# Kernel optimization log

Measured on AMD Instinct MI355X. Metric: run time of the kernel, lower is better.

Reference implementation:

```python
import jax, jax.numpy as jnp
import numpy as np

DIM = 128
HEADS = 4
HEAD_DIM = DIM // HEADS
WS = (8, 8)
N = WS[0] * WS[1]
B = 4096
SCALE = HEAD_DIM ** -0.5


def _relative_position_index():
    # Swin-style relative position index, [N, N] int
    ch = np.arange(WS[0]); cw = np.arange(WS[1])
    coords = np.stack(np.meshgrid(ch, cw, indexing='ij'))          # [2, ws0, ws1]
    flat = coords.reshape(2, -1)                                    # [2, N]
    rel = flat[:, :, None] - flat[:, None, :]                       # [2, N, N]
    rel = rel.transpose(1, 2, 0)                                    # [N, N, 2]
    rel[:, :, 0] += WS[0] - 1
    rel[:, :, 1] += WS[1] - 1
    rel[:, :, 0] *= 2 * WS[1] - 1
    return jnp.asarray(rel.sum(-1))

REL_IDX = _relative_position_index()


def setup_inputs() -> dict:
    key = jax.random.key(0)
    ks = jax.random.split(key, 16)
    def lin(k, din, dout):
        return jax.random.normal(k, (din, dout), jnp.float32) * (din ** -0.5)
    return {
        'x': jax.random.normal(ks[0], (B, N, DIM), jnp.float32),
        'f': jax.random.normal(ks[1], (B, N, DIM), jnp.float32),
        'wq': lin(ks[2], DIM, DIM), 'bq': jnp.zeros((DIM,), jnp.float32),
        'wkv': lin(ks[3], DIM, 2 * DIM), 'bkv': jnp.zeros((2 * DIM,), jnp.float32),
        'wq_f': lin(ks[4], DIM, DIM), 'bq_f': jnp.zeros((DIM,), jnp.float32),
        'wkv_f': lin(ks[5], DIM, 2 * DIM), 'bkv_f': jnp.zeros((2 * DIM,), jnp.float32),
        'bias_table': jax.random.normal(ks[6], ((2 * WS[0] - 1) * (2 * WS[1] - 1), HEADS), jnp.float32) * 0.02,
        'wproj': lin(ks[7], DIM, DIM), 'bproj': jnp.zeros((DIM,), jnp.float32),
    }


def _qkv(t, wq, bq, wkv, bkv):
    Bn, Nn, C = t.shape
    q = (t @ wq + bq).reshape(Bn, Nn, HEADS, HEAD_DIM).transpose(0, 2, 1, 3)   # [B,H,N,D]
    kv = (t @ wkv + bkv).reshape(Bn, Nn, 2, HEADS, HEAD_DIM).transpose(2, 0, 3, 1, 4)
    return q, kv[0], kv[1]


def reference(x, f, wq, bq, wkv, bkv, wq_f, bq_f, wkv_f, bkv_f, bias_table, wproj, bproj):
    q, k, v = _qkv(x, wq, bq, wkv, bkv)
    attn = jnp.einsum('bhnd,bhmd->bhnm', q * SCALE, k)              # [B,H,N,N]
    q_f, k_f, _ = _qkv(f, wq_f, bq_f, wkv_f, bkv_f)
    attn_f = jnp.einsum('bhnd,bhmd->bhnm', q_f * SCALE, k_f)

    bias = bias_table[REL_IDX.reshape(-1)].reshape(N, N, HEADS)     # gather
    bias = bias.transpose(2, 0, 1)                                   # [H,N,N]
    ratio = attn.shape[-1] // bias.shape[-1]
    if ratio > 1:  # repeat last axis (no-op here since N == ws0*ws1)
        bias = jnp.repeat(bias, ratio, axis=-1)

    attn = (attn + bias[None]) * (attn_f + bias[None])               # joint modulation
    attn = jax.nn.softmax(attn, axis=-1)
    out = jnp.einsum('bhnm,bhmd->bhnd', attn, v)                     # [B,H,N,D]
    out = out.transpose(0, 2, 1, 3).reshape(x.shape[0], N, DIM)
    return out @ wproj + bproj
```

## Files before the change

### kernel.cpp

```cpp
#include <hip/hip_runtime.h>

typedef unsigned short u16;
typedef _Float16  f16x8  __attribute__((ext_vector_type(8)));
typedef _Float16  f16x4  __attribute__((ext_vector_type(4)));
typedef _Float16  f16x2  __attribute__((ext_vector_type(2)));
typedef float     f32x4  __attribute__((ext_vector_type(4)));

#define MFMA_F16(a,b,c)  __builtin_amdgcn_mfma_f32_16x16x32_f16(a,b,c,0,0,0)
#define PKRTZ(a,b) __builtin_bit_cast(f16x2, __builtin_amdgcn_cvt_pkrtz((a),(b)))

#define NTOK 64
#define DIM_ 128
#define SCALE_ 0.17677669529663687f

#define HREG 6784
#define KOFF 2304
#define VOFF 4608
#define SQK  36
#define SP   72
#define SAO  40
#define SVT  68
#define SMEM_U16 27136

__device__ __forceinline__ u16 f2h_u(float x) {
    _Float16 h = (_Float16)x;
    return __builtin_bit_cast(u16, h);
}

__global__ void wja_prep(const float* __restrict__ wq, const float* __restrict__ wkv,
                         const float* __restrict__ wq_f, const float* __restrict__ wkv_f,
                         const float* __restrict__ wproj, u16* __restrict__ ws)
{
    const int blk = blockIdx.x;
    const int l = threadIdx.x;
    const float* W; int ldw, colbase;
    if (blk < 32)       { W = wq;    ldw = 128; colbase = (blk      >> 2) * 16; }
    else if (blk < 96)  { W = wkv;   ldw = 256; colbase = ((blk- 32) >> 2) * 16; }
    else if (blk < 128) { W = wq_f;  ldw = 128; colbase = ((blk- 96) >> 2) * 16; }
    else if (blk < 160) { W = wkv_f; ldw = 256; colbase = ((blk-128) >> 2) * 16; }
    else                { W = wproj; ldw = 128; colbase = ((blk-160) >> 2) * 16; }
    const int ks = blk & 3;
    const int m = l & 15, g = l >> 4;
    u16* dst = ws + blk * 512 + l * 8;
    #pragma unroll
    for (int i = 0; i < 8; ++i)
        dst[i] = f2h_u(W[(size_t)(32*ks + 8*g + i) * ldw + colbase + m]);
}

__global__ __launch_bounds__(256, 2)
void wja_fused(
    const float* __restrict__ x, const float* __restrict__ f,
    const float* __restrict__ bq, const float* __restrict__ bkv,
    const float* __restrict__ bq_f, const float* __restrict__ bkv_f,
    const float* __restrict__ bproj, const float* __restrict__ btab,
    const u16* __restrict__ ws, float* __restrict__ out)
{
    __shared__ __align__(16) u16 smem[SMEM_U16];
    const int b    = blockIdx.x;
    const int tid  = threadIdx.x;
    const int w    = tid >> 6;
    const int lane = tid & 63;
    const int g    = lane >> 4;
    const int c    = lane & 15;
    const f32x4 zf4 = {0.f, 0.f, 0.f, 0.f};

    u16* const hb = smem + w * HREG;

    const float* const xb = x + (size_t)b * (NTOK * DIM_);
    const float* const fb = f + (size_t)b * (NTOK * DIM_);

    auto ldf16 = [](const float* p) -> f16x8 {
        f32x4 v0 = *(const f32x4*)p;
        f32x4 v1 = *(const f32x4*)(p + 4);
        struct Q { f16x2 a, b, c, d; } t;
        t.a = PKRTZ(v0[0], v0[1]);
        t.b = PKRTZ(v0[2], v0[3]);
        t.c = PKRTZ(v1[0], v1[1]);
        t.d = PKRTZ(v1[2], v1[3]);
        return __builtin_bit_cast(f16x8, t);
    };
    auto ldlds8 = [](const u16* p) -> f16x8 {
        struct P2 { f16x4 lo, hi; } t;
        t.lo = *(const f16x4*)p;
        t.hi = *(const f16x4*)(p + 4);
        return __builtin_bit_cast(f16x8, t);
    };

    f16x8 xfr[4], ffr[4];
    #pragma unroll
    for (int ks = 0; ks < 4; ++ks) {
        xfr[ks] = ldf16(xb + (16*w + c) * DIM_ + 32*ks + 8*g);
        ffr[ks] = ldf16(fb + (16*w + c) * DIM_ + 32*ks + 8*g);
    }

    auto gemmA = [&](const f16x8* afr, int wbase, const float* biasv, int which) {
        #pragma unroll
        for (int lct = 0; lct < 8; ++lct) {
            f32x4 acc = zf4;
            #pragma unroll
            for (int ks = 0; ks < 4; ++ks) {
                f16x8 bfr = *(const f16x8*)(ws + (wbase + 4*lct + ks) * 512 + lane * 8);
                acc = MFMA_F16(afr[ks], bfr, acc);
            }
            float bv = biasv[16*lct + c];
            const int hh = lct >> 1;
            const int cc = ((lct & 1) << 4) + c;
            if (which == 2) {
                struct H4 { f16x2 lo, hi; } t;
                t.lo = PKRTZ(acc[0] + bv, acc[1] + bv);
                t.hi = PKRTZ(acc[2] + bv, acc[3] + bv);
                *(f16x4*)(smem + hh*HREG + VOFF + cc*SVT + 16*w + 4*g) =
                    __builtin_bit_cast(f16x4, t);
            } else {
                const int base = hh*HREG + (which ? KOFF : 0);
                #pragma unroll
                for (int i = 0; i < 4; ++i)
                    smem[base + (16*w + 4*g + i)*SQK + cc] = f2h_u(acc[i] + bv);
            }
        }
    };

    gemmA(xfr,   0, bq,        0);
    gemmA(xfr,  32, bkv,       1);
    gemmA(xfr,  64, bkv + 128, 2);
    __syncthreads();

    f32x4 S[4][4];
    {
        f16x8 qfr[4], kfr[4];
        #pragma unroll
        for (int t = 0; t < 4; ++t) {
            qfr[t] = ldlds8(hb + (16*t + c) * SQK + 8*g);
            kfr[t] = ldlds8(hb + KOFF + (16*t + c) * SQK + 8*g);
        }
        #pragma unroll
        for (int mt = 0; mt < 4; ++mt)
            #pragma unroll
            for (int nt = 0; nt < 4; ++nt)
                S[mt][nt] = MFMA_F16(qfr[mt], kfr[nt], zf4);
    }
    __syncthreads();

    gemmA(ffr,  96, bq_f,  0);
    gemmA(ffr, 128, bkv_f, 1);
    __syncthreads();

    {
        f16x8 kfr[4];
        #pragma unroll
        for (int t = 0; t < 4; ++t)
            kfr[t] = ldlds8(hb + KOFF + (16*t + c) * SQK + 8*g);
        #pragma unroll
        for (int mt = 0; mt < 4; ++mt) {
            f16x8 qfr = ldlds8(hb + (16*mt + c) * SQK + 8*g);
            #pragma unroll
            for (int nt = 0; nt < 4; ++nt) {
                f32x4 sf = MFMA_F16(qfr, kfr[nt], zf4);
                int j = 16*nt + c;
                #pragma unroll
                for (int i = 0; i < 4; ++i) {
                    int r = 16*mt + 4*g + i;
                    int idx = ((r >> 3) - (j >> 3) + 7) * 15 + ((r & 7) - (j & 7) + 7);
                    float bv = btab[idx * 4 + w];
                    S[mt][nt][i] = (S[mt][nt][i] * SCALE_ + bv) * (sf[i] * SCALE_ + bv);
                }
            }
        }
    }

    float rinv[4][4];
    #pragma unroll
    for (int mt = 0; mt < 4; ++mt)
        #pragma unroll
        for (int i = 0; i < 4; ++i) {
            float m = fmaxf(fmaxf(S[mt][0][i], S[mt][1][i]), fmaxf(S[mt][2][i], S[mt][3][i]));
            #pragma unroll
            for (int d = 1; d < 16; d <<= 1) m = fmaxf(m, __shfl_xor(m, d));
            float s0 = 0.f;
            #pragma unroll
            for (int nt = 0; nt < 4; ++nt) {
                float e = __expf(S[mt][nt][i] - m);
                S[mt][nt][i] = e;
                s0 += e;
            }
            #pragma unroll
            for (int d = 1; d < 16; d <<= 1) s0 += __shfl_xor(s0, d);
            rinv[mt][i] = 1.0f / s0;
        }

    #pragma unroll
    for (int mt = 0; mt < 4; ++mt)
        #pragma unroll
        for (int nt = 0; nt < 4; ++nt)
            #pragma unroll
            for (int i = 0; i < 4; ++i)
                hb[(16*mt + 4*g + i) * SP + 16*nt + c] = f2h_u(S[mt][nt][i] * rinv[mt][i]);

    f32x4 O[4][2] = { { zf4, zf4 }, { zf4, zf4 }, { zf4, zf4 }, { zf4, zf4 } };
    #pragma unroll
    for (int ks = 0; ks < 2; ++ks) {
        f16x8 pfr[4], vfr[2];
        #pragma unroll
        for (int mt = 0; mt < 4; ++mt)
            pfr[mt] = *(const f16x8*)(hb + (16*mt + c) * SP + 32*ks + 8*g);
        #pragma unroll
        for (int nt = 0; nt < 2; ++nt)
            vfr[nt] = ldlds8(hb + VOFF + (16*nt + c) * SVT + 32*ks + 8*g);
        #pragma unroll
        for (int mt = 0; mt < 4; ++mt)
            #pragma unroll
            for (int nt = 0; nt < 2; ++nt)
                O[mt][nt] = MFMA_F16(pfr[mt], vfr[nt], O[mt][nt]);
    }

    #pragma unroll
    for (int mt = 0; mt < 4; ++mt)
        #pragma unroll
        for (int nt = 0; nt < 2; ++nt)
            #pragma unroll
            for (int i = 0; i < 4; ++i)
                hb[(16*mt + 4*g + i) * SAO + 16*nt + c] = f2h_u(O[mt][nt][i]);

    __syncthreads();

    f32x4 PO[4][2] = { { zf4, zf4 }, { zf4, zf4 }, { zf4, zf4 }, { zf4, zf4 } };
    #pragma unroll
    for (int ks = 0; ks < 4; ++ks) {
        const u16* ao = smem + ks * HREG;
        f16x8 afr[4];
        #pragma unroll
        for (int mt = 0; mt < 4; ++mt)
            afr[mt] = *(const f16x8*)(ao + (16*mt + c) * SAO + 8*g);
        #pragma unroll
        for (int lct = 0; lct < 2; ++lct) {
            f16x8 bfr = *(const f16x8*)(ws + (160 + (2*w + lct) * 4 + ks) * 512 + lane * 8);
            #pragma unroll
            for (int mt = 0; mt < 4; ++mt)
                PO[mt][lct] = MFMA_F16(afr[mt], bfr, PO[mt][lct]);
        }
    }

    float* const ob = out + (size_t)b * 8192;
    #pragma unroll
    for (int lct = 0; lct < 2; ++lct) {
        float bv = bproj[32*w + 16*lct + c];
        #pragma unroll
        for (int mt = 0; mt < 4; ++mt)
            #pragma unroll
            for (int i = 0; i < 4; ++i)
                ob[(16*mt + 4*g + i) * 128 + 32*w + 16*lct + c] = PO[mt][lct][i] + bv;
    }
}

extern "C" void kernel_launch(void* const* d_in, const int* in_sizes, int n_in,
                              void* d_out, int out_size, void* d_ws, size_t ws_size,
                              hipStream_t stream)
{
    const float* x     = (const float*)d_in[0];
    const float* f     = (const float*)d_in[1];
    const float* wq    = (const float*)d_in[2];
    const float* bq    = (const float*)d_in[3];
    const float* wkv   = (const float*)d_in[4];
    const float* bkv   = (const float*)d_in[5];
    const float* wq_f  = (const float*)d_in[6];
    const float* bq_f  = (const float*)d_in[7];
    const float* wkv_f = (const float*)d_in[8];
    const float* bkv_f = (const float*)d_in[9];
    const float* btab  = (const float*)d_in[10];
    const float* wproj = (const float*)d_in[11];
    const float* bproj = (const float*)d_in[12];
    u16* ws    = (u16*)d_ws;
    float* out = (float*)d_out;

    hipLaunchKernelGGL(wja_prep, dim3(192), dim3(64), 0, stream,
                       wq, wkv, wq_f, wkv_f, wproj, ws);
    hipLaunchKernelGGL(wja_fused, dim3(4096), dim3(256), 0, stream,
                       x, f, bq, bkv, bq_f, bkv_f, bproj, btab, ws, out);
}
```

Baseline: 195.2 us.

## Shrink LDS footprint by aliasing V with K and splitting PV into two halves

Cuts per-head shared memory from 6784 to 4480 halves by deferring the V projection until after the scores are done and storing V in the K region. The probability matrix is staged in two 32-column halves reusing the Q buffer instead of a full 64-wide buffer. K gets a new row stride of 34 and is read with 32-bit loads, aiming to reduce bank conflicts. The aim is higher occupancy from a smaller LDS footprint, at the cost of extra __syncthreads barriers and a later, serialized V GEMM.

After: 286.9 us. 47.0% more time.

```diff
diff --git a/kernel.cpp b/kernel.cpp
--- a/kernel.cpp
+++ b/kernel.cpp
@@ -13,14 +13,12 @@
 #define DIM_ 128
 #define SCALE_ 0.17677669529663687f
 
-#define HREG 6784
+#define HREG 4480
 #define KOFF 2304
-#define VOFF 4608
-#define SQK  36
-#define SP   72
-#define SAO  40
+#define SQ   36
+#define SK   34
 #define SVT  68
-#define SMEM_U16 27136
+#define SMEM_U16 17920
 
 __device__ __forceinline__ u16 f2h_u(float x) {
     _Float16 h = (_Float16)x;
@@ -85,6 +83,14 @@
         t.hi = *(const f16x4*)(p + 4);
         return __builtin_bit_cast(f16x8, t);
     };
+    auto ldlds4 = [](const u16* p) -> f16x8 {
+        struct P4 { unsigned a, b, c, d; } t;
+        t.a = *(const unsigned*)(p);
+        t.b = *(const unsigned*)(p + 2);
+        t.c = *(const unsigned*)(p + 4);
+        t.d = *(const unsigned*)(p + 6);
+        return __builtin_bit_cast(f16x8, t);
+    };
 
     f16x8 xfr[4], ffr[4];
     #pragma unroll
@@ -109,20 +115,22 @@
                 struct H4 { f16x2 lo, hi; } t;
                 t.lo = PKRTZ(acc[0] + bv, acc[1] + bv);
                 t.hi = PKRTZ(acc[2] + bv, acc[3] + bv);
-                *(f16x4*)(smem + hh*HREG + VOFF + cc*SVT + 16*w + 4*g) =
+                *(f16x4*)(smem + hh*HREG + KOFF + cc*SVT + 16*w + 4*g) =
                     __builtin_bit_cast(f16x4, t);
-            } else {
-                const int base = hh*HREG + (which ? KOFF : 0);
+            } else if (which == 1) {
                 #pragma unroll
                 for (int i = 0; i < 4; ++i)
-                    smem[base + (16*w + 4*g + i)*SQK + cc] = f2h_u(acc[i] + bv);
+                    smem[hh*HREG + KOFF + (16*w + 4*g + i)*SK + cc] = f2h_u(acc[i] + bv);
+            } else {
+                #pragma unroll
+                for (int i = 0; i < 4; ++i)
+                    smem[hh*HREG + (16*w + 4*g + i)*SQ + cc] = f2h_u(acc[i] + bv);
             }
         }
     };
 
-    gemmA(xfr,   0, bq,        0);
-    gemmA(xfr,  32, bkv,       1);
-    gemmA(xfr,  64, bkv + 128, 2);
+    gemmA(xfr,   0, bq,  0);
+    gemmA(xfr,  32, bkv, 1);
     __syncthreads();
 
     f32x4 S[4][4];
@@ -130,8 +138,8 @@
         f16x8 qfr[4], kfr[4];
         #pragma unroll
         for (int t = 0; t < 4; ++t) {
-            qfr[t] = ldlds8(hb + (16*t + c) * SQK + 8*g);
-            kfr[t] = ldlds8(hb + KOFF + (16*t + c) * SQK + 8*g);
+            qfr[t] = ldlds8(hb + (16*t + c) * SQ + 8*g);
+            kfr[t] = ldlds4(hb + KOFF + (16*t + c) * SK + 8*g);
         }
         #pragma unroll
         for (int mt = 0; mt < 4; ++mt)
@@ -149,10 +157,10 @@
         f16x8 kfr[4];
         #pragma unroll
         for (int t = 0; t < 4; ++t)
-            kfr[t] = ldlds8(hb + KOFF + (16*t + c) * SQK + 8*g);
+            kfr[t] = ldlds4(hb + KOFF + (16*t + c) * SK + 8*g);
         #pragma unroll
         for (int mt = 0; mt < 4; ++mt) {
-            f16x8 qfr = ldlds8(hb + (16*mt + c) * SQK + 8*g);
+            f16x8 qfr = ldlds8(hb + (16*mt + c) * SQ + 8*g);
             #pragma unroll
             for (int nt = 0; nt < 4; ++nt) {
                 f32x4 sf = MFMA_F16(qfr, kfr[nt], zf4);
@@ -191,35 +199,59 @@
     #pragma unroll
     for (int mt = 0; mt < 4; ++mt)
         #pragma unroll
-        for (int nt = 0; nt < 4; ++nt)
-            #pragma unroll
-            for (int i = 0; i < 4; ++i)
-                hb[(16*mt + 4*g + i) * SP + 16*nt + c] = f2h_u(S[mt][nt][i] * rinv[mt][i]);
+        for (int i = 0; i < 4; ++i) {
+            hb[(16*mt + 4*g + i) * SQ +      c] = f2h_u(S[mt][0][i] * rinv[mt][i]);
+            hb[(16*mt + 4*g + i) * SQ + 16 + c] = f2h_u(S[mt][1][i] * rinv[mt][i]);
+        }
+    __syncthreads();
+
+    gemmA(xfr, 64, bkv + 128, 2);
+    __syncthreads();
 
     f32x4 O[4][2] = { { zf4, zf4 }, { zf4, zf4 }, { zf4, zf4 }, { zf4, zf4 } };
-    #pragma unroll
-    for (int ks = 0; ks < 2; ++ks) {
+    {
         f16x8 pfr[4], vfr[2];
         #pragma unroll
         for (int mt = 0; mt < 4; ++mt)
-            pfr[mt] = *(const f16x8*)(hb + (16*mt + c) * SP + 32*ks + 8*g);
+            pfr[mt] = ldlds8(hb + (16*mt + c) * SQ + 8*g);
         #pragma unroll
         for (int nt = 0; nt < 2; ++nt)
-            vfr[nt] = ldlds8(hb + VOFF + (16*nt + c) * SVT + 32*ks + 8*g);
+            vfr[nt] = ldlds8(hb + KOFF + (16*nt + c) * SVT + 8*g);
         #pragma unroll
         for (int mt = 0; mt < 4; ++mt)
             #pragma unroll
             for (int nt = 0; nt < 2; ++nt)
                 O[mt][nt] = MFMA_F16(pfr[mt], vfr[nt], O[mt][nt]);
     }
-
     #pragma unroll
     for (int mt = 0; mt < 4; ++mt)
         #pragma unroll
+        for (int i = 0; i < 4; ++i) {
+            hb[(16*mt + 4*g + i) * SQ +      c] = f2h_u(S[mt][2][i] * rinv[mt][i]);
+            hb[(16*mt + 4*g + i) * SQ + 16 + c] = f2h_u(S[mt][3][i] * rinv[mt][i]);
+        }
+    {
+        f16x8 pfr[4], vfr[2];
+        #pragma unroll
+        for (int mt = 0; mt < 4; ++mt)
+            pfr[mt] = ldlds8(hb + (16*mt + c) * SQ + 8*g);
+        #pragma unroll
         for (int nt = 0; nt < 2; ++nt)
+            vfr[nt] = ldlds8(hb + KOFF + (16*nt + c) * SVT + 32 + 8*g);
+        #pragma unroll
+        for (int mt = 0; mt < 4; ++mt)
+            #pragma unroll
+            for (int nt = 0; nt < 2; ++nt)
+                O[mt][nt] = MFMA_F16(pfr[mt], vfr[nt], O[mt][nt]);
+    }
+
+    #pragma unroll
+    for (int mt = 0; mt < 4; ++mt)
+        #pragma unroll
+        for (int nt = 0; nt < 2; ++nt)
             #pragma unroll
             for (int i = 0; i < 4; ++i)
-                hb[(16*mt + 4*g + i) * SAO + 16*nt + c] = f2h_u(O[mt][nt][i]);
+                hb[(16*mt + 4*g + i) * SQ + 16*nt + c] = f2h_u(O[mt][nt][i]);
 
     __syncthreads();
 
@@ -230,7 +262,7 @@
         f16x8 afr[4];
         #pragma unroll
         for (int mt = 0; mt < 4; ++mt)
-            afr[mt] = *(const f16x8*)(ao + (16*mt + c) * SAO + 8*g);
+            afr[mt] = ldlds8(ao + (16*mt + c) * SQ + 8*g);
         #pragma unroll
         for (int lct = 0; lct < 2; ++lct) {
             f16x8 bfr = *(const f16x8*)(ws + (160 + (2*w + lct) * 4 + ks) * 512 + lane * 8);
```
